# Kernel optimization log

Hardware: AMD Instinct MI355X
Metric: run time of the kernel (lower is better)

The kernel has to match this reference:

```python
import jax, jax.numpy as jnp
import numpy as np
from jax import lax

INPUT_SIZE = 64
HIDDEN_SIZE = 4096
OUTPUT_SIZE = 16
SEQ_LEN = 4096
SPECTRAL_RADIUS = 0.95
LEAKY_RATE = 0.9
INPUT_SCALING = 1.0
FEEDBACK_SCALING = 0.1
SPARSITY = 0.1


def setup_inputs() -> dict:
    key = jax.random.key(0)
    ks = jax.random.split(key, 7)
    X = jax.random.normal(ks[0], (SEQ_LEN, INPUT_SIZE), dtype=jnp.float32)
    W_in = jax.random.normal(ks[1], (HIDDEN_SIZE, INPUT_SIZE), dtype=jnp.float32) * INPUT_SCALING
    # sparse reservoir matrix, scaled so spectral radius ~ SPECTRAL_RADIUS
    dense = jax.random.normal(ks[2], (HIDDEN_SIZE, HIDDEN_SIZE), dtype=jnp.float32)
    mask = (jax.random.uniform(ks[3], (HIDDEN_SIZE, HIDDEN_SIZE)) < SPARSITY).astype(jnp.float32)
    # circular-law estimate of spectral radius for sparse gaussian: sqrt(density*N)
    scale = SPECTRAL_RADIUS / np.sqrt(SPARSITY * HIDDEN_SIZE)
    W_res = dense * mask * scale
    b = jax.random.normal(ks[4], (HIDDEN_SIZE,), dtype=jnp.float32)
    W_fb = jax.random.normal(ks[5], (HIDDEN_SIZE, OUTPUT_SIZE), dtype=jnp.float32) * FEEDBACK_SCALING
    W_out = jax.random.normal(ks[6], (OUTPUT_SIZE, HIDDEN_SIZE), dtype=jnp.float32) * 0.01
    return {"X": X, "W_in": W_in, "W_res": W_res, "b": b, "W_fb": W_fb, "W_out": W_out}


def reference(X, W_in, W_res, b, W_fb, W_out):
    """ESN with feedback + leaky integration; Force readout (inference: y = W_out @ s).
    Returns (results [T, O], outputs [T, H]) matching ESNForce.forward."""
    H = W_res.shape[0]
    O = W_out.shape[0]

    def step(carry, x_t):
        s, y = carry  # previous state [H], previous output [O]
        pre = W_in @ x_t + W_res @ s + b + W_fb @ y
        s_new = (1.0 - LEAKY_RATE) * s + LEAKY_RATE * jnp.tanh(pre)
        y_new = W_out @ s_new
        return (s_new, y_new), (y_new, s_new)

    init = (jnp.zeros((H,), dtype=X.dtype), jnp.zeros((O,), dtype=X.dtype))
    _, (results, outputs) = lax.scan(step, init, X)
    return results, outputs
```

## Files before the change

### kernel.cpp

```cpp
#include <hip/hip_runtime.h>
#include <cstdint>

#define NBLK 128
#define BLOCK 1024
#define ROWS 32
#define HDIM 4096
#define IDIM 64
#define ODIM 16
#define TSTEPS 4096
#define PAD 576
#define GMAX 18
#define LEAK 0.9f
#define SUN 16
#define YU 8
#define SPAD 34

typedef float f32x4 __attribute__((ext_vector_type(4)));

__global__ void init_ws(float* ws) {
    int i = blockIdx.x * blockDim.x + threadIdx.x;
    if (i < (2 * NBLK * SUN + 2 * NBLK * YU) * 4) ws[i] = 0.0f;
}

__global__ __launch_bounds__(BLOCK) void esn_kernel(
    const float* __restrict__ X,
    const float* __restrict__ Win,
    const float* __restrict__ Wres,
    const float* __restrict__ bvec,
    const float* __restrict__ Wfb,
    const float* __restrict__ Wout,
    float* __restrict__ out,
    float* __restrict__ sx,
    float* __restrict__ yx)
{
    __shared__ float          ell_val[ROWS][PAD];
    __shared__ unsigned short ell_idx[ROWS][PAD];
    __shared__ __align__(16) float s_lds[2][NBLK*SPAD];
    __shared__ float          win_lds[ROWS][IDIM];
    __shared__ float          wfb_lds[ROWS][ODIM];
    __shared__ __align__(8)  float wout_lds[ROWS][ODIM];
    __shared__ float          b_lds[ROWS];
    __shared__ float          x_lds[IDIM];
    __shared__ float          y_lds[ODIM];
    __shared__ __align__(16) float snew_lds[ROWS];
    __shared__ int            nnz_lds[ROWS];
    __shared__ int            rnds_lds[ROWS];
    __shared__ unsigned char  bankCnt[ROWS][32];
    __shared__ unsigned char  grpCnt[ROWS][GMAX];

    const int tid   = threadIdx.x;
    const int blk   = blockIdx.x;
    const int rbase = blk * ROWS;
    const int rowB  = tid >> 5;
    const int lB    = tid & 31;
    const int wv    = tid >> 6;
    const int ln    = tid & 63;

    for (int i = tid; i < ROWS * PAD; i += BLOCK) {
        ell_val[i / PAD][i % PAD] = 0.0f;
        ell_idx[i / PAD][i % PAD] = 0;
    }
    for (int i = tid; i < ROWS * 32; i += BLOCK) bankCnt[i >> 5][i & 31] = 0;
    for (int i = tid; i < ROWS * GMAX; i += BLOCK) grpCnt[i / GMAX][i % GMAX] = 0;

    for (int rr = wv * 2; rr < wv * 2 + 2; ++rr) {
        const float* wrow = Wres + (size_t)(rbase + rr) * HDIM;
        int cnt = 0;
        for (int c0 = 0; c0 < HDIM; c0 += 64)
            cnt += __popcll(__ballot(wrow[c0 + ln] != 0.0f));
        if (ln == 0) {
            int nz = cnt < PAD ? cnt : PAD;
            nnz_lds[rr] = nz;
            int gu = (nz + 31) >> 5;
            if (gu < 1) gu = 1;
            if (gu > GMAX) gu = GMAX;
            rnds_lds[rr] = (gu + 1) >> 1;
        }
    }
    __syncthreads();

    if (ln == 0 || ln == 32) {
        const int row = wv * 2 + (ln >> 5);
        const int nz  = nnz_lds[row];
        int gu = (nz + 31) >> 5;
        if (gu < 1) gu = 1;
        if (gu > GMAX) gu = GMAX;
        const float* wrow = Wres + (size_t)(rbase + row) * HDIM;
        int placed = 0;
        for (int c = 0; c < HDIM && placed < nz; ++c) {
            const float w = wrow[c];
            if (w != 0.0f) {
                const int pidx = c + 2 * (c >> 5);
                const int b = pidx & 31;
                const int r = bankCnt[row][b];
                bankCnt[row][b] = (unsigned char)(r + 1);
                int g = r % gu;
                int p = grpCnt[row][g];
                int guard = 0;
                while (p >= 32 && guard < GMAX) {
                    g = (g + 1 == gu) ? 0 : g + 1;
                    p = grpCnt[row][g];
                    ++guard;
                }
                if (p >= 32) break;
                grpCnt[row][g] = (unsigned char)(p + 1);
                const int slot = ((g >> 1) << 6) + 2 * p + (g & 1);
                ell_val[row][slot] = w;
                ell_idx[row][slot] = (unsigned short)pidx;
                ++placed;
            }
        }
    }

    for (int i = tid; i < ROWS * IDIM; i += BLOCK)
        win_lds[i >> 6][i & 63] = Win[(size_t)(rbase + (i >> 6)) * IDIM + (i & 63)];
    for (int i = tid; i < ROWS * ODIM; i += BLOCK)
        wfb_lds[i >> 4][i & 15] = Wfb[(size_t)(rbase + (i >> 4)) * ODIM + (i & 15)];
    for (int i = tid; i < ROWS * ODIM; i += BLOCK)
        wout_lds[i >> 4][i & 15] = Wout[(size_t)(i & 15) * HDIM + rbase + (i >> 4)];
    if (tid < ROWS) b_lds[tid] = bvec[rbase + tid];

    {
        float* sz = &s_lds[0][0];
        for (int i = tid; i < 2 * NBLK * SPAD; i += BLOCK) sz[i] = 0.0f;
    }
    if (tid < ODIM) y_lds[tid] = 0.0f;
    if (tid >= 64 && tid < 128) x_lds[tid - 64] = X[tid - 64];
    __syncthreads();

    float* out_res = out;
    float* out_s   = out + (size_t)TSTEPS * ODIM;
    const int RB = rnds_lds[rowB];

    for (int t = 0; t < TSTEPS; ++t) {
        const unsigned tu = (unsigned)(t + 1);
        const float tagf = __uint_as_float(tu);
        const int cur = t & 1, nxt = cur ^ 1;

        {
            const float* sc = s_lds[cur];
            float a0 = 0.0f, a1 = 0.0f;
            for (int k = 0; k < RB; ++k) {
                const int e = (k << 6) + (lB << 1);
                const float2  v  = *(const float2*)&ell_val[rowB][e];
                const ushort2 ix = *(const ushort2*)&ell_idx[rowB][e];
                a0 += v.x * sc[ix.x];
                a1 += v.y * sc[ix.y];
            }
            float acc = a0 + a1;
            acc += win_lds[rowB][lB] * x_lds[lB] + win_lds[rowB][lB + 32] * x_lds[lB + 32];
            if (lB < ODIM) acc += wfb_lds[rowB][lB] * y_lds[lB];
            acc += __shfl_xor(acc, 16, 32);
            acc += __shfl_xor(acc, 8, 32);
            acc += __shfl_xor(acc, 4, 32);
            acc += __shfl_xor(acc, 2, 32);
            acc += __shfl_xor(acc, 1, 32);
            float sn = 0.0f;
            if (lB == 0) {
                const float pre = acc + b_lds[rowB];
                sn = (1.0f - LEAK) * sc[blk * SPAD + rowB] + LEAK * tanhf(pre);
                snew_lds[rowB] = sn;
            }
            const float sn1 = __shfl(sn, 32);
            if (ln == 0) {
                f32x4 v; v.x = sn; v.y = sn1; v.z = 0.0f; v.w = tagf;
                float* dst = sx + (((size_t)cur * NBLK + blk) * SUN + wv) * 4;
                asm volatile("global_store_dwordx4 %0, %1, off sc0 sc1"
                             :: "v"(dst), "v"(v) : "memory");
                float2 o2; o2.x = sn; o2.y = sn1;
                *(float2*)(out_s + (size_t)t * HDIM + rbase + 2 * wv) = o2;
            }
        }
        __syncthreads();

        if (wv == 0) {
            if (ln < YU) {
                float a0 = 0.0f, a1 = 0.0f;
                #pragma unroll
                for (int r = 0; r < ROWS; ++r) {
                    const float2 w = *(const float2*)&wout_lds[r][2 * ln];
                    a0 += w.x * snew_lds[r];
                    a1 += w.y * snew_lds[r];
                }
                f32x4 v; v.x = a0; v.y = a1; v.z = tagf; v.w = 0.0f;
                float* dst = yx + (((size_t)cur * NBLK + blk) * YU + ln) * 4;
                asm volatile("global_store_dwordx4 %0, %1, off sc0 sc1"
                             :: "v"(dst), "v"(v) : "memory");
            }
        } else if (wv == 1) {
            if (t + 1 < TSTEPS) x_lds[ln] = X[(size_t)(t + 1) * IDIM + ln];
            const int u  = ln & 7;
            const int pg = ln >> 3;
            const float* yb = yx + (size_t)cur * NBLK * YU * 4;
            f32x4 w0,w1,w2,w3,w4,w5,w6,w7,w8,w9,w10,w11,w12,w13,w14,w15;
            for (;;) {
                #define YL(i) asm volatile("global_load_dwordx4 %0, %1, off sc0 sc1" \
                    : "=v"(w##i) : "v"(yb + (((pg << 4) + i) * YU + u) * 4));
                YL(0) YL(1) YL(2) YL(3) YL(4) YL(5) YL(6) YL(7)
                YL(8) YL(9) YL(10) YL(11) YL(12) YL(13) YL(14) YL(15)
                #undef YL
                asm volatile("s_waitcnt vmcnt(0)" ::: "memory");
                __builtin_amdgcn_sched_barrier(0);
                bool ok = __float_as_uint(w0.z) == tu  && __float_as_uint(w1.z) == tu
                       && __float_as_uint(w2.z) == tu  && __float_as_uint(w3.z) == tu
                       && __float_as_uint(w4.z) == tu  && __float_as_uint(w5.z) == tu
                       && __float_as_uint(w6.z) == tu  && __float_as_uint(w7.z) == tu
                       && __float_as_uint(w8.z) == tu  && __float_as_uint(w9.z) == tu
                       && __float_as_uint(w10.z) == tu && __float_as_uint(w11.z) == tu
                       && __float_as_uint(w12.z) == tu && __float_as_uint(w13.z) == tu
                       && __float_as_uint(w14.z) == tu && __float_as_uint(w15.z) == tu;
                if (__all(ok)) break;
            }
            float acc0 = ((w0.x + w1.x) + (w2.x + w3.x)) + ((w4.x + w5.x) + (w6.x + w7.x))
                       + ((w8.x + w9.x) + (w10.x + w11.x)) + ((w12.x + w13.x) + (w14.x + w15.x));
            float acc1 = ((w0.y + w1.y) + (w2.y + w3.y)) + ((w4.y + w5.y) + (w6.y + w7.y))
                       + ((w8.y + w9.y) + (w10.y + w11.y)) + ((w12.y + w13.y) + (w14.y + w15.y));
            acc0 += __shfl_xor(acc0, 8);  acc1 += __shfl_xor(acc1, 8);
            acc0 += __shfl_xor(acc0, 16); acc1 += __shfl_xor(acc1, 16);
            acc0 += __shfl_xor(acc0, 32); acc1 += __shfl_xor(acc1, 32);
            if (ln < 8) {
                if (t + 1 < TSTEPS) { y_lds[2 * u] = acc0; y_lds[2 * u + 1] = acc1; }
                if (blk == 0) {
                    out_res[(size_t)t * ODIM + 2 * u]     = acc0;
                    out_res[(size_t)t * ODIM + 2 * u + 1] = acc1;
                }
            }
        } else {
            if (t + 1 < TSTEPS) {
                const int wi    = wv - 2;
                const int start = (wi < 2) ? wi * 10 : 20 + (wi - 2) * 9;
                const int count = (wi < 2) ? 10 : 9;
                const int U     = count * SUN;
                const float* sb = sx + ((size_t)cur * NBLK + start) * SUN * 4;
                const int g0 = ln, g1 = ln + 64, g2 = ln + 128;
                const bool h1 = g1 < U, h2 = g2 < U;
                f32x4 v0, v1, v2;
                for (;;) {
                    asm volatile("global_load_dwordx4 %0, %1, off sc0 sc1"
                                 : "=v"(v0) : "v"(sb + (size_t)g0 * 4));
                    if (h1)
                        asm volatile("global_load_dwordx4 %0, %1, off sc0 sc1"
                                     : "=v"(v1) : "v"(sb + (size_t)g1 * 4));
                    if (h2)
                        asm volatile("global_load_dwordx4 %0, %1, off sc0 sc1"
                                     : "=v"(v2) : "v"(sb + (size_t)g2 * 4));
                    asm volatile("s_waitcnt vmcnt(0)" ::: "memory");
                    __builtin_amdgcn_sched_barrier(0);
                    bool ok = (__float_as_uint(v0.w) == tu)
                           && (!h1 || __float_as_uint(v1.w) == tu)
                           && (!h2 || __float_as_uint(v2.w) == tu);
                    if (__all(ok)) break;
                }
                float* sd = s_lds[nxt];
                {   const int pp = start + (g0 >> 4), u = g0 & 15;
                    float2 s2; s2.x = v0.x; s2.y = v0.y;
                    *(float2*)&sd[pp * SPAD + 2 * u] = s2; }
                if (h1) {
                    const int pp = start + (g1 >> 4), u = g1 & 15;
                    float2 s2; s2.x = v1.x; s2.y = v1.y;
                    *(float2*)&sd[pp * SPAD + 2 * u] = s2; }
                if (h2) {
                    const int pp = start + (g2 >> 4), u = g2 & 15;
                    float2 s2; s2.x = v2.x; s2.y = v2.y;
                    *(float2*)&sd[pp * SPAD + 2 * u] = s2; }
            }
        }
        __syncthreads();
    }
}

extern "C" void kernel_launch(void* const* d_in, const int* in_sizes, int n_in,
                              void* d_out, int out_size, void* d_ws, size_t ws_size,
                              hipStream_t stream) {
    (void)in_sizes; (void)n_in; (void)out_size; (void)ws_size;
    const float* X    = (const float*)d_in[0];
    const float* Win  = (const float*)d_in[1];
    const float* Wres = (const float*)d_in[2];
    const float* b    = (const float*)d_in[3];
    const float* Wfb  = (const float*)d_in[4];
    const float* Wout = (const float*)d_in[5];
    float* out = (float*)d_out;
    float* sx  = (float*)d_ws;
    float* yx  = (float*)d_ws + 2 * NBLK * SUN * 4;

    const int words = (2 * NBLK * SUN + 2 * NBLK * YU) * 4;
    init_ws<<<(words + 255) / 256, 256, 0, stream>>>((float*)d_ws);
    esn_kernel<<<NBLK, BLOCK, 0, stream>>>(X, Win, Wres, b, Wfb, Wout, out, sx, yx);
}
```

Baseline: 19.46 ms.

## Replace mid-step block barrier with per-wave LDS flags and partial W_out sums

Each wave now computes its two new states, forms a partial W_out product for its two rows in LDS, and raises a per-wave release flag. Wave 0 spins on those flags instead of a full __syncthreads before reducing the 16 partials into the block's y contribution. x and y buffers become double-buffered so the prefetch of the next step cannot race with readers of the current step. This removes one block-wide barrier per timestep from the serial recurrence, at the cost of spin-waiting in wave 0 and relying on the remaining barrier elsewhere for correctness.

```diff
diff --git a/kernel.cpp b/kernel.cpp
--- a/kernel.cpp
+++ b/kernel.cpp
@@ -40,9 +40,10 @@
     __shared__ float          wfb_lds[ROWS][ODIM];
     __shared__ __align__(8)  float wout_lds[ROWS][ODIM];
     __shared__ float          b_lds[ROWS];
-    __shared__ float          x_lds[IDIM];
-    __shared__ float          y_lds[ODIM];
-    __shared__ __align__(16) float snew_lds[ROWS];
+    __shared__ float          x_lds[2][IDIM];
+    __shared__ float          y_lds[2][ODIM];
+    __shared__ __align__(8)  float ytmp[16][18];
+    __shared__ unsigned       done[16];
     __shared__ int            nnz_lds[ROWS];
     __shared__ int            rnds_lds[ROWS];
     __shared__ unsigned char  bankCnt[ROWS][32];
@@ -62,6 +63,7 @@
     }
     for (int i = tid; i < ROWS * 32; i += BLOCK) bankCnt[i >> 5][i & 31] = 0;
     for (int i = tid; i < ROWS * GMAX; i += BLOCK) grpCnt[i / GMAX][i % GMAX] = 0;
+    if (tid < 16) done[tid] = 0u;
 
     for (int rr = wv * 2; rr < wv * 2 + 2; ++rr) {
         const float* wrow = Wres + (size_t)(rbase + rr) * HDIM;
@@ -124,8 +126,8 @@
         float* sz = &s_lds[0][0];
         for (int i = tid; i < 2 * NBLK * SPAD; i += BLOCK) sz[i] = 0.0f;
     }
-    if (tid < ODIM) y_lds[tid] = 0.0f;
-    if (tid >= 64 && tid < 128) x_lds[tid - 64] = X[tid - 64];
+    if (tid < ODIM) y_lds[0][tid] = 0.0f;
+    if (tid >= 64 && tid < 128) x_lds[0][tid - 64] = X[tid - 64];
     __syncthreads();
 
     float* out_res = out;
@@ -148,39 +150,46 @@
                 a1 += v.y * sc[ix.y];
             }
             float acc = a0 + a1;
-            acc += win_lds[rowB][lB] * x_lds[lB] + win_lds[rowB][lB + 32] * x_lds[lB + 32];
-            if (lB < ODIM) acc += wfb_lds[rowB][lB] * y_lds[lB];
+            acc += win_lds[rowB][lB] * x_lds[cur][lB]
+                 + win_lds[rowB][lB + 32] * x_lds[cur][lB + 32];
+            if (lB < ODIM) acc += wfb_lds[rowB][lB] * y_lds[cur][lB];
             acc += __shfl_xor(acc, 16, 32);
             acc += __shfl_xor(acc, 8, 32);
             acc += __shfl_xor(acc, 4, 32);
             acc += __shfl_xor(acc, 2, 32);
             acc += __shfl_xor(acc, 1, 32);
-            float sn = 0.0f;
-            if (lB == 0) {
-                const float pre = acc + b_lds[rowB];
-                sn = (1.0f - LEAK) * sc[blk * SPAD + rowB] + LEAK * tanhf(pre);
-                snew_lds[rowB] = sn;
-            }
-            const float sn1 = __shfl(sn, 32);
+            const float pre = acc + b_lds[rowB];
+            const float snAll = (1.0f - LEAK) * sc[blk * SPAD + rowB] + LEAK * tanhf(pre);
+            const float sn0 = __shfl(snAll, 0);
+            const float sn1 = __shfl(snAll, 32);
+            if (ln < 16)
+                ytmp[wv][ln] = wout_lds[2 * wv][ln] * sn0 + wout_lds[2 * wv + 1][ln] * sn1;
             if (ln == 0) {
-                f32x4 v; v.x = sn; v.y = sn1; v.z = 0.0f; v.w = tagf;
+                f32x4 v; v.x = sn0; v.y = sn1; v.z = 0.0f; v.w = tagf;
                 float* dst = sx + (((size_t)cur * NBLK + blk) * SUN + wv) * 4;
                 asm volatile("global_store_dwordx4 %0, %1, off sc0 sc1"
                              :: "v"(dst), "v"(v) : "memory");
-                float2 o2; o2.x = sn; o2.y = sn1;
+                float2 o2; o2.x = sn0; o2.y = sn1;
                 *(float2*)(out_s + (size_t)t * HDIM + rbase + 2 * wv) = o2;
-            }
-        }
-        __syncthreads();
+                __hip_atomic_store(&done[wv], tu, __ATOMIC_RELEASE,
+                                   __HIP_MEMORY_SCOPE_WORKGROUP);
+            }
+        }
 
         if (wv == 0) {
+            for (;;) {
+                unsigned f = (ln < 16)
+                    ? __hip_atomic_load(&done[ln], __ATOMIC_ACQUIRE, __HIP_MEMORY_SCOPE_WORKGROUP)
+                    : tu;
+                if (__all(f >= tu)) break;
+            }
             if (ln < YU) {
                 float a0 = 0.0f, a1 = 0.0f;
                 #pragma unroll
-                for (int r = 0; r < ROWS; ++r) {
-                    const float2 w = *(const float2*)&wout_lds[r][2 * ln];
-                    a0 += w.x * snew_lds[r];
-                    a1 += w.y * snew_lds[r];
+                for (int w = 0; w < 16; ++w) {
+                    const float2 p = *(const float2*)&ytmp[w][2 * ln];
+                    a0 += p.x;
+                    a1 += p.y;
                 }
                 f32x4 v; v.x = a0; v.y = a1; v.z = tagf; v.w = 0.0f;
                 float* dst = yx + (((size_t)cur * NBLK + blk) * YU + ln) * 4;
@@ -188,7 +197,7 @@
                              :: "v"(dst), "v"(v) : "memory");
             }
         } else if (wv == 1) {
-            if (t + 1 < TSTEPS) x_lds[ln] = X[(size_t)(t + 1) * IDIM + ln];
+            if (t + 1 < TSTEPS) x_lds[nxt][ln] = X[(size_t)(t + 1) * IDIM + ln];
             const int u  = ln & 7;
             const int pg = ln >> 3;
             const float* yb = yx + (size_t)cur * NBLK * YU * 4;
@@ -219,7 +228,7 @@
             acc0 += __shfl_xor(acc0, 16); acc1 += __shfl_xor(acc1, 16);
             acc0 += __shfl_xor(acc0, 32); acc1 += __shfl_xor(acc1, 32);
             if (ln < 8) {
-                if (t + 1 < TSTEPS) { y_lds[2 * u] = acc0; y_lds[2 * u + 1] = acc1; }
+                if (t + 1 < TSTEPS) { y_lds[nxt][2 * u] = acc0; y_lds[nxt][2 * u + 1] = acc1; }
                 if (blk == 0) {
                     out_res[(size_t)t * ODIM + 2 * u]     = acc0;
                     out_res[(size_t)t * ODIM + 2 * u + 1] = acc1;
```

Result: faster. 18.87 ms (median of 2 runs) (-3.0%).
